# Kernel optimization log

Measured on AMD Instinct MI355X. Metric: run time of the kernel, lower is better.

Reference implementation:

```python
import jax, jax.numpy as jnp
import numpy as np
import math

# ---- module config (from init_kwargs) ----
IRREPS = [(0, 8), (1, 8), (2, 8), (3, 8), (4, 8)]  # (l, multiplicity)
MAX_M = max(l for l, _ in IRREPS)
TOTAL_DIM = sum(m * (2 * l + 1) for l, m in IRREPS)  # 200
BATCH, CHANNELS = 2048, 128

# ---- constant per-l change-of-axis matrices A_l = D_real^l(Rx(-pi/2)) ----
# Wigner ZYZ decomposition in the real spherical-harmonic basis:
#   D^l(a,b,g) = Z(a) @ A_l @ Z(b) @ A_l^T @ Z(g)
# where Z(theta) is the sparse real Z-rotation (cos/sin m*theta blocks).

def _small_d(l, beta):
    d = np.zeros((2 * l + 1, 2 * l + 1))
    for mp in range(-l, l + 1):
        for m in range(-l, l + 1):
            pref = math.sqrt(math.factorial(l + mp) * math.factorial(l - mp)
                             * math.factorial(l + m) * math.factorial(l - m))
            tot = 0.0
            for s in range(max(0, m - mp), min(l + m, l - mp) + 1):
                den = (math.factorial(l + m - s) * math.factorial(s)
                       * math.factorial(mp - m + s) * math.factorial(l - mp - s))
                tot += ((-1.0) ** (mp - m + s) / den
                        * math.cos(beta / 2) ** (2 * l + m - mp - 2 * s)
                        * math.sin(beta / 2) ** (mp - m + 2 * s))
            d[mp + l, m + l] = pref * tot
    return d

def _U(l):
    # complex->real spherical harmonic change of basis
    U = np.zeros((2 * l + 1, 2 * l + 1), dtype=np.complex128)
    U[l, l] = 1.0
    for m in range(1, l + 1):
        U[l + m, l + m] = (-1.0) ** m / math.sqrt(2)
        U[l + m, l - m] = 1.0 / math.sqrt(2)
        U[l - m, l - m] = 1j / math.sqrt(2)
        U[l - m, l + m] = -1j * (-1.0) ** m / math.sqrt(2)
    return U

def _A(l):
    # real Wigner-D of Rx(-pi/2) = Rz(-pi/2) Ry(-pi/2) Rz(pi/2)
    a, b, g = -np.pi / 2, -np.pi / 2, np.pi / 2
    mv = np.arange(-l, l + 1)
    Dc = np.exp(-1j * mv[:, None] * a) * _small_d(l, b) * np.exp(-1j * mv[None, :] * g)
    U = _U(l)
    return np.real(U @ Dc @ U.conj().T)

A_MATS = {l: jnp.asarray(_A(l), dtype=jnp.float32) for l in sorted({l for l, _ in IRREPS})}


def _sincos(key, batch):
    theta = jax.random.uniform(key, (batch,), minval=0.0, maxval=2 * np.pi)
    m = jnp.arange(MAX_M + 1, dtype=jnp.float32)          # (max_m+1,)
    mt = theta[:, None] * m[None, :]                       # (B, max_m+1)
    return jnp.stack([jnp.sin(mt), jnp.cos(mt)], axis=-1).astype(jnp.float32)


def setup_inputs() -> dict:
    key = jax.random.key(0)
    k0, k1, k2, k3 = jax.random.split(key, 4)
    return {
        "input": jax.random.normal(k0, (BATCH, TOTAL_DIM, CHANNELS), dtype=jnp.float32),
        "sincos_alpha": _sincos(k1, BATCH),
        "sincos_beta": _sincos(k2, BATCH),
        "sincos_gamma": _sincos(k3, BATCH),
    }


def _zrot(x, sincos, l):
    # x: (B, mult, 2l+1, C); sincos: (B, max_m+1, 2) with [...,0]=sin(m t), [...,1]=cos(m t)
    # out[m] = cos(m t) x[m] + sin(m t) x[-m]   (m = -l..l; sin odd, cos even)
    m = jnp.arange(-l, l + 1)
    am = jnp.abs(m)
    cos = sincos[:, am, 1]                                  # (B, 2l+1)
    sin = jnp.sign(m).astype(x.dtype) * sincos[:, am, 0]    # (B, 2l+1)
    return cos[:, None, :, None] * x + sin[:, None, :, None] * x[:, :, ::-1, :]


def reference(input, sincos_alpha, sincos_beta, sincos_gamma):
    B, _, C = input.shape
    outs = []
    off = 0
    for l, mult in IRREPS:
        d = 2 * l + 1
        seg = input[:, off:off + mult * d, :].reshape(B, mult, d, C)
        off += mult * d
        A = A_MATS[l]
        y = _zrot(seg, sincos_gamma, l)
        y = jnp.einsum('ij,bmjc->bmic', A.T, y)
        y = _zrot(y, sincos_beta, l)
        y = jnp.einsum('ij,bmjc->bmic', A, y)
        y = _zrot(y, sincos_alpha, l)
        outs.append(y.reshape(B, mult * d, C))
    return jnp.concatenate(outs, axis=1)
```

## Files before the change

kernel.cpp:

```cpp
#include <hip/hip_runtime.h>


#define NBATCH 2048

__device__ __forceinline__ double small_d_elem(int L, int jp, int jm) {
  int mp = jp - L, m = jm - L;
  double f[10];
  f[0] = 1.0;
  for (int i = 1; i < 10; ++i) f[i] = f[i - 1] * (double)i;
  double pref = sqrt(f[L + mp] * f[L - mp] * f[L + m] * f[L - m]);
  const double c  =  0.70710678118654752440;
  const double sn = -0.70710678118654752440;
  double tot = 0.0;
  int s0 = (m - mp) > 0 ? (m - mp) : 0;
  int s1 = (L + m) < (L - mp) ? (L + m) : (L - mp);
  for (int s = s0; s <= s1; ++s) {
    double den  = f[L + m - s] * f[s] * f[mp - m + s] * f[L - mp - s];
    double term = (((mp - m + s) & 1) ? -1.0 : 1.0) / den;
    int e1 = 2 * L + m - mp - 2 * s;
    int e2 = mp - m + 2 * s;
    double p1 = 1.0, p2 = 1.0;
    for (int t = 0; t < e1; ++t) p1 *= c;
    for (int t = 0; t < e2; ++t) p2 *= sn;
    tot += term * p1 * p2;
  }
  return pref * tot;
}

__device__ __forceinline__ int urow_entries(int L, int p, int* c, double* r, int* ph) {
  const double s2 = 0.70710678118654752440;
  int m = p - L;
  if (m == 0) { c[0] = L; r[0] = 1.0; ph[0] = 0; return 1; }
  if (m > 0) {
    c[0] = L + m; r[0] = ((m & 1) ? -s2 : s2); ph[0] = 0;
    c[1] = L - m; r[1] = s2;                   ph[1] = 0;
    return 2;
  }
  int mu = -m;
  c[0] = L - mu; r[0] = s2;                    ph[0] = 1;
  c[1] = L + mu; r[1] = ((mu & 1) ? s2 : -s2); ph[1] = 1;
  return 2;
}

template <int L, int RB, int RO>
__device__ __forceinline__ void apply_block(const float4* __restrict__ ib,
                                            float4* __restrict__ ob,
                                            const float* __restrict__ Rsm, int g) {
  constexpr int D = 2 * L + 1;
  const float4* ip = ib + (RB + g * D) * 32;
  float4* op = ob + (RB + g * D) * 32;
  const float* R = Rsm + RO;
  float4 x[D];
#pragma unroll
  for (int j = 0; j < D; ++j) x[j] = ip[j * 32];
#pragma unroll
  for (int i = 0; i < D; ++i) {
    float r = R[i * D];
    float4 a;
    a.x = r * x[0].x; a.y = r * x[0].y; a.z = r * x[0].z; a.w = r * x[0].w;
#pragma unroll
    for (int j = 1; j < D; ++j) {
      r = R[i * D + j];
      a.x = fmaf(r, x[j].x, a.x);
      a.y = fmaf(r, x[j].y, a.y);
      a.z = fmaf(r, x[j].z, a.z);
      a.w = fmaf(r, x[j].w, a.w);
    }
    op[i * 32] = a;
  }
}

__global__ __launch_bounds__(256, 4) void wigner_fused_kernel(
    const float* __restrict__ in, const float* __restrict__ sa,
    const float* __restrict__ sb, const float* __restrict__ sg,
    float* __restrict__ out) {
  __shared__ double dsm[165];
  __shared__ float Asm[165];
  __shared__ float Msm[165];
  __shared__ float Rsm[165];

  const int t = threadIdx.x;
  const int b = blockIdx.x;

  int L = 0, off = 0;
  if (t >= 84) { L = 4; off = 84; }
  else if (t >= 35) { L = 3; off = 35; }
  else if (t >= 10) { L = 2; off = 10; }
  else if (t >= 1)  { L = 1; off = 1; }
  const int D = 2 * L + 1;
  const int loc = t - off;
  const int i = loc / D;
  const int j = loc - i * D;

  if (t < 165) dsm[t] = small_d_elem(L, i, j);
  __syncthreads();

  if (t < 165) {
    int c1[2], ph1[2], c2[2], ph2[2];
    double r1[2], r2[2];
    int n1 = urow_entries(L, i, c1, r1, ph1);
    int n2 = urow_entries(L, j, c2, r2, ph2);
    double acc = 0.0;
    for (int a = 0; a < n1; ++a)
      for (int bq = 0; bq < n2; ++bq) {
        int tp = ((c1[a] - c2[bq]) + ph1[a] - ph2[bq] + 12) & 3;
        double v = r1[a] * r2[bq] * dsm[off + c1[a] * D + c2[bq]];
        if (tp == 0) acc += v;
        else if (tp == 2) acc -= v;
      }
    Asm[t] = (float)acc;
  }
  __syncthreads();

  if (t < 165) {
    float acc = 0.0f;
    for (int ii = 0; ii < D; ++ii) {
      int mm = ii - L;
      int am = mm < 0 ? -mm : mm;
      float sgn = (float)((mm > 0) - (mm < 0));
      float cb = sb[b * 10 + am * 2 + 1];
      float sv = sgn * sb[b * 10 + am * 2 + 0];
      acc += Asm[off + i * D + ii] *
             (cb * Asm[off + j * D + ii] + sv * Asm[off + j * D + (2 * L - ii)]);
    }
    Msm[t] = acc;
  }
  __syncthreads();

  if (t < 165) {
    int p = i, k = j;
    int mmp = p - L, amp = mmp < 0 ? -mmp : mmp;
    float sgp = (float)((mmp > 0) - (mmp < 0));
    float cap = sa[b * 10 + amp * 2 + 1];
    float sav = sgp * sa[b * 10 + amp * 2 + 0];
    int mmk = k - L, amk = mmk < 0 ? -mmk : mmk;
    float sgk = (float)((mmk > 0) - (mmk < 0));
    float cgk = sg[b * 10 + amk * 2 + 1];
    float sgv = sgk * sg[b * 10 + amk * 2 + 0];
    float m00 = Msm[off + p * D + k];
    float m01 = Msm[off + p * D + (2 * L - k)];
    float m10 = Msm[off + (2 * L - p) * D + k];
    float m11 = Msm[off + (2 * L - p) * D + (2 * L - k)];
    Rsm[t] = cap * (cgk * m00 - sgv * m01) + sav * (cgk * m10 - sgv * m11);
  }
  __syncthreads();

  const int g = t >> 5;
  const int q = t & 31;
  const float4* ib = (const float4*)in + (size_t)b * 6400 + q;
  float4* ob = (float4*)out + (size_t)b * 6400 + q;
  apply_block<0, 0,   0 >(ib, ob, Rsm, g);
  apply_block<1, 8,   1 >(ib, ob, Rsm, g);
  apply_block<2, 32,  10>(ib, ob, Rsm, g);
  apply_block<3, 72,  35>(ib, ob, Rsm, g);
  apply_block<4, 128, 84>(ib, ob, Rsm, g);
}

extern "C" void kernel_launch(void* const* d_in, const int* in_sizes, int n_in,
                              void* d_out, int out_size, void* d_ws, size_t ws_size,
                              hipStream_t stream) {
  const float* in = (const float*)d_in[0];
  const float* sa = (const float*)d_in[1];
  const float* sb = (const float*)d_in[2];
  const float* sg = (const float*)d_in[3];
  float* out = (float*)d_out;

  wigner_fused_kernel<<<dim3(NBATCH), 256, 0, stream>>>(in, sa, sb, sg, out);
}
```

Before: 358.0 us.

## Precompute constant A matrices on host via kernarg and prefetch input early

The constant change-of-axis matrices A_l are now computed once on the host in double precision and passed as a by-value kernel argument. The kernel reads them from the kernarg segment pointer instead of computing Wigner small-d and basis-change values per block in double precision with an extra barrier. The input loads for the l=0 and l=1 segments are also issued before the setup phase so their latency overlaps the shared-memory matrix construction. This relies on the struct being at offset zero of the kernarg segment, and adds a large kernel argument plus per-launch host work.

```diff
diff --git a/kernel.cpp b/kernel.cpp
--- a/kernel.cpp
+++ b/kernel.cpp
@@ -1,9 +1,10 @@
 #include <hip/hip_runtime.h>
+#include <math.h>
 
 
 #define NBATCH 2048
 
-__device__ __forceinline__ double small_d_elem(int L, int jp, int jm) {
+__host__ __device__ __forceinline__ double small_d_elem_hd(int L, int jp, int jm) {
   int mp = jp - L, m = jm - L;
   double f[10];
   f[0] = 1.0;
@@ -27,7 +28,7 @@
   return pref * tot;
 }
 
-__device__ __forceinline__ int urow_entries(int L, int p, int* c, double* r, int* ph) {
+__host__ __device__ __forceinline__ int urow_entries_hd(int L, int p, int* c, double* r, int* ph) {
   const double s2 = 0.70710678118654752440;
   int m = p - L;
   if (m == 0) { c[0] = L; r[0] = 1.0; ph[0] = 0; return 1; }
@@ -40,6 +41,35 @@
   c[0] = L - mu; r[0] = s2;                    ph[0] = 1;
   c[1] = L + mu; r[1] = ((mu & 1) ? s2 : -s2); ph[1] = 1;
   return 2;
+}
+
+struct APack { float a[165]; };
+
+static void host_compute_A(APack* out) {
+  const int offs[5] = {0, 1, 10, 35, 84};
+  for (int L = 0; L <= 4; ++L) {
+    const int D = 2 * L + 1;
+    double dsm[81];
+    for (int jp = 0; jp < D; ++jp)
+      for (int jm = 0; jm < D; ++jm)
+        dsm[jp * D + jm] = small_d_elem_hd(L, jp, jm);
+    for (int p = 0; p < D; ++p)
+      for (int q = 0; q < D; ++q) {
+        int c1[2], ph1[2], c2[2], ph2[2];
+        double r1[2], r2[2];
+        int n1 = urow_entries_hd(L, p, c1, r1, ph1);
+        int n2 = urow_entries_hd(L, q, c2, r2, ph2);
+        double acc = 0.0;
+        for (int a = 0; a < n1; ++a)
+          for (int bq = 0; bq < n2; ++bq) {
+            int tp = ((c1[a] - c2[bq]) + ph1[a] - ph2[bq] + 12) & 3;
+            double v = r1[a] * r2[bq] * dsm[c1[a] * D + c2[bq]];
+            if (tp == 0) acc += v;
+            else if (tp == 2) acc -= v;
+          }
+        out->a[offs[L] + p * D + q] = (float)acc;
+      }
+  }
 }
 
 template <int L, int RB, int RO>
@@ -70,17 +100,31 @@
   }
 }
 
-__global__ __launch_bounds__(256, 4) void wigner_fused_kernel(
+__global__ __launch_bounds__(256, 4) void wigner_fused2(
+    APack Ap,
     const float* __restrict__ in, const float* __restrict__ sa,
     const float* __restrict__ sb, const float* __restrict__ sg,
     float* __restrict__ out) {
-  __shared__ double dsm[165];
+  (void)Ap;
   __shared__ float Asm[165];
   __shared__ float Msm[165];
   __shared__ float Rsm[165];
 
   const int t = threadIdx.x;
   const int b = blockIdx.x;
+  const int g = t >> 5;
+  const int q = t & 31;
+
+  const float4* ib = (const float4*)in + (size_t)b * 6400 + q;
+  float4* ob = (float4*)out + (size_t)b * 6400 + q;
+
+  float4 p0 = ib[g * 32];
+  float4 p1[3];
+#pragma unroll
+  for (int j = 0; j < 3; ++j) p1[j] = ib[(8 + g * 3 + j) * 32];
+
+  const float* Ak = (const float*)__builtin_amdgcn_kernarg_segment_ptr();
+  if (t < 165) Asm[t] = Ak[t];
 
   int L = 0, off = 0;
   if (t >= 84) { L = 4; off = 84; }
@@ -91,25 +135,6 @@
   const int loc = t - off;
   const int i = loc / D;
   const int j = loc - i * D;
-
-  if (t < 165) dsm[t] = small_d_elem(L, i, j);
-  __syncthreads();
-
-  if (t < 165) {
-    int c1[2], ph1[2], c2[2], ph2[2];
-    double r1[2], r2[2];
-    int n1 = urow_entries(L, i, c1, r1, ph1);
-    int n2 = urow_entries(L, j, c2, r2, ph2);
-    double acc = 0.0;
-    for (int a = 0; a < n1; ++a)
-      for (int bq = 0; bq < n2; ++bq) {
-        int tp = ((c1[a] - c2[bq]) + ph1[a] - ph2[bq] + 12) & 3;
-        double v = r1[a] * r2[bq] * dsm[off + c1[a] * D + c2[bq]];
-        if (tp == 0) acc += v;
-        else if (tp == 2) acc -= v;
-      }
-    Asm[t] = (float)acc;
-  }
   __syncthreads();
 
   if (t < 165) {
@@ -145,12 +170,30 @@
   }
   __syncthreads();
 
-  const int g = t >> 5;
-  const int q = t & 31;
-  const float4* ib = (const float4*)in + (size_t)b * 6400 + q;
-  float4* ob = (float4*)out + (size_t)b * 6400 + q;
-  apply_block<0, 0,   0 >(ib, ob, Rsm, g);
-  apply_block<1, 8,   1 >(ib, ob, Rsm, g);
+  {
+    float r0 = Rsm[0];
+    float4 a;
+    a.x = r0 * p0.x; a.y = r0 * p0.y; a.z = r0 * p0.z; a.w = r0 * p0.w;
+    ob[g * 32] = a;
+  }
+  {
+    const float* R1 = Rsm + 1;
+#pragma unroll
+    for (int i2 = 0; i2 < 3; ++i2) {
+      float r = R1[i2 * 3];
+      float4 a;
+      a.x = r * p1[0].x; a.y = r * p1[0].y; a.z = r * p1[0].z; a.w = r * p1[0].w;
+#pragma unroll
+      for (int j2 = 1; j2 < 3; ++j2) {
+        r = R1[i2 * 3 + j2];
+        a.x = fmaf(r, p1[j2].x, a.x);
+        a.y = fmaf(r, p1[j2].y, a.y);
+        a.z = fmaf(r, p1[j2].z, a.z);
+        a.w = fmaf(r, p1[j2].w, a.w);
+      }
+      ob[(8 + g * 3 + i2) * 32] = a;
+    }
+  }
   apply_block<2, 32,  10>(ib, ob, Rsm, g);
   apply_block<3, 72,  35>(ib, ob, Rsm, g);
   apply_block<4, 128, 84>(ib, ob, Rsm, g);
@@ -165,5 +208,8 @@
   const float* sg = (const float*)d_in[3];
   float* out = (float*)d_out;
 
-  wigner_fused_kernel<<<dim3(NBATCH), 256, 0, stream>>>(in, sa, sb, sg, out);
-}
+  APack Ap;
+  host_compute_A(&Ap);
+
+  wigner_fused2<<<dim3(NBATCH), 256, 0, stream>>>(Ap, in, sa, sb, sg, out);
+}
```

Result: no change. 353.8 us (-1.2%).
